# Kernel tuning notes

Measured on AMD Instinct MI355X. Metric: run time of the kernel, lower is better.

## Reference

```python
import jax, jax.numpy as jnp
import numpy as np

HID = 128      # hidden_dim
NR = 8         # num_radial
MAXL = 4       # max_angular -> 2*MAXL+1 = 9 circular harmonic features
CUT = 10.0     # cutoff
EDGE_IN = 2 * HID + NR + (2 * MAXL + 1)  # 273


def setup_inputs() -> dict:
    key = jax.random.key(0)
    ks = jax.random.split(key, 16)
    B, N = 2, 512

    def rn(k, shape, scale=0.05):
        return jax.random.normal(k, shape, dtype=jnp.float32) * scale

    return {
        "h": rn(ks[0], (B, N, HID), 1.0),
        "pos": rn(ks[1], (B, N, 2), 2.0),
        "vel": rn(ks[2], (B, N, 2), 1.0),
        # edge_net: Linear(273,256) -> SiLU -> Linear(256,128)
        "ew1": rn(ks[3], (EDGE_IN, 2 * HID)), "eb1": jnp.zeros(2 * HID, jnp.float32),
        "ew2": rn(ks[4], (2 * HID, HID)), "eb2": jnp.zeros(HID, jnp.float32),
        # coord_net: Linear(128,128) -> SiLU -> Linear(128,1)
        "cw1": rn(ks[5], (HID, HID)), "cb1": jnp.zeros(HID, jnp.float32),
        "cw2": rn(ks[6], (HID, 1)), "cb2": jnp.zeros(1, jnp.float32),
        # node_net: Linear(256,128) -> SiLU -> Linear(128,128)
        "nw1": rn(ks[7], (2 * HID, HID)), "nb1": jnp.zeros(HID, jnp.float32),
        "nw2": rn(ks[8], (HID, HID)), "nb2": jnp.zeros(HID, jnp.float32),
        # LayerNorm
        "ln_g": jnp.ones(HID, jnp.float32), "ln_b": jnp.zeros(HID, jnp.float32),
    }


def reference(h, pos, vel, ew1, eb1, ew2, eb2, cw1, cb1, cw2, cb2,
              nw1, nb1, nw2, nb2, ln_g, ln_b):
    B, N, _ = h.shape
    # all-pairs geometry: [B, N, N, 2]
    pos_diff = pos[:, :, None, :] - pos[:, None, :, :]
    dist = jnp.sqrt(jnp.sum(pos_diff * pos_diff, axis=-1))        # [B,N,N]
    direction = pos_diff / (dist[..., None] + 1e-8)

    # Gaussian radial basis on [0, cutoff]
    centers = jnp.linspace(0.0, CUT, NR).astype(h.dtype)
    width = CUT / NR
    radial = jnp.exp(-jnp.square((dist[..., None] - centers) / width))  # [B,N,N,NR]

    # smooth cosine cutoff
    cutoff = jnp.where(dist < CUT, 0.5 * (jnp.cos(jnp.pi * dist / CUT) + 1.0), 0.0)
    cutoff = cutoff[..., None]                                     # [B,N,N,1]

    # circular harmonics: [1, cos(m t), sin(m t)] m=1..MAXL -> 9 features
    theta = jnp.arctan2(direction[..., 1], direction[..., 0])
    m = jnp.arange(1, MAXL + 1, dtype=h.dtype)
    mt = theta[..., None] * m
    angular = jnp.concatenate(
        [jnp.ones_like(theta)[..., None], jnp.cos(mt), jnp.sin(mt)], axis=-1)

    h_i = jnp.broadcast_to(h[:, :, None, :], (B, N, N, HID))
    h_j = jnp.broadcast_to(h[:, None, :, :], (B, N, N, HID))
    edge_input = jnp.concatenate([h_i, h_j, radial, angular], axis=-1)  # [B,N,N,273]

    # edge MLP (dropout = identity in eval)
    e = jax.nn.silu(edge_input @ ew1 + eb1) @ ew2 + eb2            # [B,N,N,HID]
    e = e * cutoff

    # coordinate weights and position/velocity updates
    cw = (jax.nn.silu(e @ cw1 + cb1) @ cw2 + cb2)[..., 0]          # [B,N,N]
    upd = jnp.sum(pos_diff * cw[..., None], axis=2)                # [B,N,2]
    pos_out = pos + upd
    vel_out = vel + 0.1 * upd

    # message aggregation + node update
    msg_agg = jnp.sum(e, axis=2)                                   # [B,N,HID]
    node_input = jnp.concatenate([h, msg_agg], axis=-1)
    h_new = jax.nn.silu(node_input @ nw1 + nb1) @ nw2 + nb2

    # residual + LayerNorm
    x = h + h_new
    mu = jnp.mean(x, axis=-1, keepdims=True)
    var = jnp.var(x, axis=-1, keepdims=True)
    h_out = (x - mu) / jnp.sqrt(var + 1e-5) * ln_g + ln_b
    return h_out, pos_out, vel_out
```

## Files before the change

kernel.cpp:

```cpp
#include <hip/hip_runtime.h>
#include <math.h>

#define HID 128
#define NN 512
#define NNODE 1024
#define CUTR 10.0f

#define WS_A    0
#define WS_N1T  262144
#define WS_N2T  294912
#define WS_B12  393216
#define SBMT_OFF  786688
#define SE2T_OFF  (SBMT_OFF + 262144)
#define SW12T_OFF (SE2T_OFF + 32768)
#define SW1G_OFF  (SW12T_OFF + 32768)

#define OUT_POS 131072
#define OUT_VEL 133120

typedef __attribute__((ext_vector_type(8)))  short short8;
typedef __attribute__((ext_vector_type(4)))  unsigned short ushort4v;
typedef __attribute__((ext_vector_type(8)))  __bf16 bf16x8;
typedef __attribute__((ext_vector_type(16))) float float16;

__device__ __forceinline__ float silu_f(float x) {
  return x * __builtin_amdgcn_rcpf(1.f + __expf(-x));
}
__device__ __forceinline__ short f2bf(float x) {
  return __builtin_bit_cast(short, (__bf16)x);
}
__device__ __forceinline__ float bf2f(unsigned short u) {
  union { unsigned u; float f; } v; v.u = ((unsigned)u) << 16;
  return v.f;
}
__device__ __forceinline__ bf16x8 as_bf(short8 s) {
  return __builtin_bit_cast(bf16x8, s);
}
__device__ __forceinline__ float16 zero16() {
  float16 z;
#pragma unroll
  for (int r = 0; r < 16; ++r) z[r] = 0.f;
  return z;
}

__global__ __launch_bounds__(256)
void k01_prep(const float* __restrict__ h, const float* __restrict__ ew1,
              const float* __restrict__ eb1, const float* __restrict__ ew2,
              const float* __restrict__ cw1, const float* __restrict__ eb2,
              const float* __restrict__ nw1, const float* __restrict__ nw2,
              float* __restrict__ ws, unsigned short* __restrict__ wsU) {
  int blk = blockIdx.x;
  int t = threadIdx.x;
  if (blk < 1024) {
    __shared__ float sh_h[HID];
    const int node = blk;
    if (t < HID) sh_h[t] = h[node*HID + t];
    __syncthreads();
    const int c = t;
    float a = eb1[c] + ew1[264*256 + c];
    float bm = 0.f;
#pragma unroll 8
    for (int k = 0; k < HID; ++k) {
      float hk = sh_h[k];
      a  += hk * ew1[k*256 + c];
      bm += hk * ew1[(128+k)*256 + c];
    }
    ws[WS_A + node*256 + c] = a;
    const int b = node >> 9, j = node & 511;
    const int chunk = j >> 5, jr = j & 31;
    const int e = jr & 3, hlw = (jr >> 2) & 1, g = jr >> 3;
    wsU[SBMT_OFF + b*131072 + chunk*8192 + g*2048 + (c*2 + hlw)*4 + e] =
        (unsigned short)f2bf(bm);
  } else {
    int idx = (blk - 1024) * 256 + t;
    if (idx < 32768) {
      int d = idx & 127, cp = idx >> 7;
      float s = 0.f;
#pragma unroll 4
      for (int c = 0; c < 128; ++c) s += ew2[cp*128 + c] * cw1[c*128 + d];
      int sg = cp >> 4, hlw = (cp >> 3) & 1, e = cp & 7;
      wsU[SW12T_OFF + sg*2048 + d*16 + hlw*8 + e] = (unsigned short)f2bf(s);
    } else if (idx < 65536) {
      int i2 = idx - 32768; int c = i2 >> 8, k = i2 & 255;
      wsU[SE2T_OFF + c*256 + k] = (unsigned short)f2bf(ew2[k*HID + c]);
    } else if (idx < 69632) {
      int i3 = idx - 65536; int c = i3 >> 4, f = i3 & 15;
      int row = (f < 8) ? (256 + f) : (257 + f);
      wsU[SW1G_OFF + c*16 + f] = (unsigned short)f2bf(ew1[row*256 + c]);
    } else if (idx < 69760) {
      int d = idx - 69632;
      float s = 0.f;
#pragma unroll 4
      for (int c = 0; c < 128; ++c) s += eb2[c] * cw1[c*128 + d];
      ws[WS_B12 + d] = s;
    } else if (idx < 102528) {
      int i4 = idx - 69760; int d = i4 >> 8, k = i4 & 255;
      ws[WS_N1T + d*256 + k] = nw1[k*HID + d];
    } else if (idx < 118912) {
      int i5 = idx - 102528; int d = i5 >> 7, k = i5 & 127;
      ws[WS_N2T + d*128 + k] = nw2[k*HID + d];
    }
  }
}

__global__ __launch_bounds__(256)
void k3_edge(const float* __restrict__ pos, const float* __restrict__ vel,
             const float* __restrict__ h,
             const float* __restrict__ cb1, const float* __restrict__ cw2,
             const float* __restrict__ cb2, const float* __restrict__ eb2,
             const float* __restrict__ nb1, const float* __restrict__ nb2,
             const float* __restrict__ lng, const float* __restrict__ lnb,
             float* __restrict__ ws, float* __restrict__ out) {
  const short* wsS = (const short*)ws;
  const unsigned short* wsU = (const unsigned short*)ws;
  __shared__ __align__(16) short shH[2][32*256];
  __shared__ float shsum[256];
  __shared__ float shred[12];
  __shared__ float4 shTbl[128];
  __shared__ __align__(16) float2 shPos[NN];
  __shared__ float shCut[32];

  const int t = threadIdx.x;
  const int w = t >> 6, l = t & 63, lo = l & 31, hl = l >> 5, hl4 = hl * 4;
  const int node = blockIdx.x;
  const int b = node >> 9;
  const int bN = b * NN;

  const bf16x8 wg0 = as_bf(*(const short8*)(wsS + SW1G_OFF + (64*w + lo)*16 + hl*8));
  const bf16x8 wg1 = as_bf(*(const short8*)(wsS + SW1G_OFF + (64*w + 32 + lo)*16 + hl*8));

  const float a0   = ws[WS_A + node*256 + 64*w + lo];
  const float a1   = ws[WS_A + node*256 + 64*w + 32 + lo];
  const float cb2c16 = cb2[0] * (16.f/128.f);
  const float pix  = pos[node*2], piy = pos[node*2+1];

  ((float4*)shPos)[t] = ((const float4*)(pos + 2*bN))[t];
  if (t < 128) shTbl[t] = make_float4(ws[WS_B12 + t], cb1[t], cw2[t], 0.f);
  __syncthreads();

  float hs0 = 0.f, hs1 = 0.f;
  float cs = 0.f;
  float S = 0.f, SX = 0.f, SY = 0.f;
  float cutv, pjx, pjy;
  float cutv_n, pjx_n, pjy_n;

  auto phase1 = [&](int jbw, int bufsel) {
    const int jb = jbw & (NN - 1);
    const int chunk = jb >> 5;
    const float2 pj = shPos[jb + lo];
    pjx_n = pj.x; pjy_n = pj.y;
    const float dx = pix - pjx_n, dy = piy - pjy_n;
    const float d = sqrtf(dx*dx + dy*dy);
    cutv_n = (d < CUTR) ? 0.5f*(__cosf((float)M_PI*(1.f/CUTR)*d) + 1.f) : 0.f;
    if (jbw >= NN) cutv_n = 0.f;
    if (hl == 0) shCut[lo] = cutv_n;
    short8 gs;
    if (hl == 0) {
#pragma unroll
      for (int k = 0; k < 8; ++k) {
        float ctr = (CUTR * (float)k) / 7.0f;
        float tt = (d - ctr) * 0.8f;
        gs[k] = f2bf(__expf(-tt*tt));
      }
    } else {
      float invd = __builtin_amdgcn_rcpf(d + 1e-8f);
      float c1 = dx * invd, s1 = dy * invd;
      if (d == 0.f) { c1 = 1.f; s1 = 0.f; }
      float c2 = c1*c1 - s1*s1, s2 = 2.f*s1*c1;
      float c3 = c2*c1 - s2*s1, s3 = s2*c1 + c2*s1;
      float c4 = c3*c1 - s3*s1, s4 = s3*c1 + c3*s1;
      gs[0]=f2bf(c1); gs[1]=f2bf(c2); gs[2]=f2bf(c3); gs[3]=f2bf(c4);
      gs[4]=f2bf(s1); gs[5]=f2bf(s2); gs[6]=f2bf(s3); gs[7]=f2bf(s4);
    }
    const bf16x8 gf = as_bf(gs);
    short* shb = &shH[bufsel][0];
#pragma unroll
    for (int ct = 0; ct < 2; ++ct) {
      const int colg = 64*w + 32*ct + lo;
      const float av = ct ? a1 : a0;
      const unsigned short* bt =
          wsU + SBMT_OFF + b*131072 + chunk*8192 + (colg*2 + hl)*4;
      float16 ci;
#pragma unroll
      for (int g = 0; g < 4; ++g) {
        ushort4v v4 = *(const ushort4v*)(bt + g*2048);
        ci[4*g+0] = bf2f(v4[0]) + av;
        ci[4*g+1] = bf2f(v4[1]) + av;
        ci[4*g+2] = bf2f(v4[2]) + av;
        ci[4*g+3] = bf2f(v4[3]) + av;
      }
      ci = __builtin_amdgcn_mfma_f32_32x32x16_bf16(gf, ct ? wg1 : wg0, ci, 0, 0, 0);
      const int ck = colg >> 3;
      float hacc = 0.f;
#pragma unroll
      for (int r = 0; r < 16; ++r) {
        int row = (r&3) + 8*(r>>2) + hl4;
        float sv = silu_f(ci[r]);
        hacc += shCut[row] * sv;
        shb[row*256 + (((ck ^ row) & 31) << 3) + (colg & 7)] = f2bf(sv);
      }
      if (ct) hs1 += hacc; else hs0 += hacc;
    }
  };

  phase1(0, 0);
  cutv = cutv_n; pjx = pjx_n; pjy = pjy_n;
  __syncthreads();

  for (int k = 0; k < 16; ++k) {
    cs += cutv;

    float16 acc2 = zero16();
    {
      const short* wp = wsS + SW12T_OFF + (32*w + lo)*16 + hl*8;
      const short* shb = &shH[k & 1][0];
#pragma unroll 4
      for (int s = 0; s < 16; ++s) {
        bf16x8 wv = as_bf(*(const short8*)(wp + s*2048));
        const int ck = 2*s + hl;
        bf16x8 af = as_bf(*(const short8*)(shb + lo*256 + (((ck ^ lo) & 31) << 3)));
        acc2 = __builtin_amdgcn_mfma_f32_32x32x16_bf16(wv, af, acc2, 0, 0, 0);
      }
    }

    phase1((k + 1) * 32, (k + 1) & 1);

    {
      float psum = 0.f;
#pragma unroll
      for (int r = 0; r < 16; ++r) {
        const float4 cst = shTbl[32*w + (r&3) + 8*(r>>2) + hl4];
        psum += silu_f(cutv * (acc2[r] + cst.x) + cst.y) * cst.z;
      }
      psum += cb2c16;
      S += psum;
      SX += psum * pjx;
      SY += psum * pjy;
    }

    cutv = cutv_n; pjx = pjx_n; pjy = pjy_n;
    __syncthreads();
  }

  hs0 += __shfl_xor(hs0, 32);
  hs1 += __shfl_xor(hs1, 32);
  if (hl == 0) {
    shsum[64*w + lo] = hs0;
    shsum[64*w + 32 + lo] = hs1;
  }

  float cutsum = cs;
#pragma unroll
  for (int m = 1; m < 32; m <<= 1) cutsum += __shfl_xor(cutsum, m, 32);

#pragma unroll
  for (int off = 32; off > 0; off >>= 1) {
    S  += __shfl_xor(S, off);
    SX += __shfl_xor(SX, off);
    SY += __shfl_xor(SY, off);
  }
  if (l == 0) { shred[w] = S; shred[4 + w] = SX; shred[8 + w] = SY; }
  __syncthreads();

  float* shIn  = (float*)&shH[0][0];
  float* shHid = shIn + 256;
  float* pm    = (float*)&shH[1][0];
  const int d  = t & 127, half = t >> 7;

  {
    const short* er = wsS + SE2T_OFF + d*256 + half*128;
    const float* ss = shsum + half*128;
    float m = 0.f;
#pragma unroll 4
    for (int kk = 0; kk < 16; ++kk) {
      short8 v = *(const short8*)(er + kk*8);
      const float4 s0 = *(const float4*)(ss + kk*8);
      const float4 s1 = *(const float4*)(ss + kk*8 + 4);
      m += bf2f((unsigned short)v[0])*s0.x + bf2f((unsigned short)v[1])*s0.y
         + bf2f((unsigned short)v[2])*s0.z + bf2f((unsigned short)v[3])*s0.w
         + bf2f((unsigned short)v[4])*s1.x + bf2f((unsigned short)v[5])*s1.y
         + bf2f((unsigned short)v[6])*s1.z + bf2f((unsigned short)v[7])*s1.w;
    }
    pm[t] = m;
  }
  if (t == 0) {
    float St  = shred[0] + shred[1] + shred[2]  + shred[3];
    float SXt = shred[4] + shred[5] + shred[6]  + shred[7];
    float SYt = shred[8] + shred[9] + shred[10] + shred[11];
    float updx = pix*St - SXt, updy = piy*St - SYt;
    out[OUT_POS + node*2+0] = pix + updx;
    out[OUT_POS + node*2+1] = piy + updy;
    out[OUT_VEL + node*2+0] = vel[node*2+0] + 0.1f*updx;
    out[OUT_VEL + node*2+1] = vel[node*2+1] + 0.1f*updy;
  }
  __syncthreads();

  if (t < HID) {
    shIn[t]       = h[node*HID + t];
    shIn[HID + t] = pm[t] + pm[t + 128] + eb2[t] * cutsum;
  }
  __syncthreads();

  {
    const float* wr = ws + WS_N1T + d*256 + half*128;
    const float* si = shIn + half*128;
    float s = 0.f;
#pragma unroll 4
    for (int kk = 0; kk < 32; ++kk) {
      float4 wv = *(const float4*)(wr + kk*4);
      float4 iv = *(const float4*)(si + kk*4);
      s += wv.x*iv.x + wv.y*iv.y + wv.z*iv.z + wv.w*iv.w;
    }
    __syncthreads();
    pm[t] = s;
  }
  __syncthreads();
  if (t < HID) shHid[t] = silu_f(nb1[t] + pm[t] + pm[t + 128]);
  __syncthreads();

  {
    const float* wr = ws + WS_N2T + d*128 + half*64;
    const float* si = shHid + half*64;
    float s = 0.f;
#pragma unroll 4
    for (int kk = 0; kk < 16; ++kk) {
      float4 wv = *(const float4*)(wr + kk*4);
      float4 iv = *(const float4*)(si + kk*4);
      s += wv.x*iv.x + wv.y*iv.y + wv.z*iv.z + wv.w*iv.w;
    }
    pm[t] = s;
  }
  __syncthreads();

  float x = 0.f;
  if (t < HID) {
    x = shIn[t] + nb2[t] + pm[t] + pm[t + 128];
    float v1 = x, v2 = x*x;
#pragma unroll
    for (int off = 32; off > 0; off >>= 1) {
      v1 += __shfl_down(v1, off);
      v2 += __shfl_down(v2, off);
    }
    if (l == 0) { shred[w] = v1; shred[2 + w] = v2; }
  }
  __syncthreads();
  if (t < HID) {
    float mu  = (shred[0] + shred[1]) * (1.f/HID);
    float var = (shred[2] + shred[3]) * (1.f/HID) - mu*mu;
    float inv = 1.f / sqrtf(var + 1e-5f);
    out[node*HID + t] = (x - mu) * inv * lng[t] + lnb[t];
  }
}

extern "C" void kernel_launch(void* const* d_in, const int* in_sizes, int n_in,
                              void* d_out, int out_size, void* d_ws, size_t ws_size,
                              hipStream_t stream) {
  (void)in_sizes; (void)n_in; (void)out_size; (void)ws_size;
  const float* h   = (const float*)d_in[0];
  const float* pos = (const float*)d_in[1];
  const float* vel = (const float*)d_in[2];
  const float* ew1 = (const float*)d_in[3];
  const float* eb1 = (const float*)d_in[4];
  const float* ew2 = (const float*)d_in[5];
  const float* eb2 = (const float*)d_in[6];
  const float* cw1 = (const float*)d_in[7];
  const float* cb1 = (const float*)d_in[8];
  const float* cw2 = (const float*)d_in[9];
  const float* cb2 = (const float*)d_in[10];
  const float* nw1 = (const float*)d_in[11];
  const float* nb1 = (const float*)d_in[12];
  const float* nw2 = (const float*)d_in[13];
  const float* nb2 = (const float*)d_in[14];
  const float* lng = (const float*)d_in[15];
  const float* lnb = (const float*)d_in[16];
  float* out = (float*)d_out;
  float* ws  = (float*)d_ws;
  unsigned short* wsU = (unsigned short*)d_ws;

  hipLaunchKernelGGL(k01_prep, dim3(1489), dim3(256), 0, stream,
                     h, ew1, eb1, ew2, cw1, eb2, nw1, nw2, ws, wsU);
  hipLaunchKernelGGL(k3_edge, dim3(NNODE), dim3(256), 0, stream,
                     pos, vel, h, cb1, cw2, cb2, eb2,
                     nb1, nb2, lng, lnb, ws, out);
}
```

Measured before the change: 263.1 us.

## Compute per-node edge-layer projections in prep kernel with split-bf16 MFMA

The prep kernel's per-node projection of h through the first edge-layer weights used one block per node with scalar FP32 loops. It now uses 128 blocks in which each wave computes a 32x32 output tile with bf16 MFMA instructions. Each operand is split into high and low bf16 parts and three products are summed to approximate FP32 accuracy. This cuts the prep grid from 1489 to 593 blocks and reduces redundant weight reads, at the cost of small precision differences and a more intricate output layout mapping.

```diff
diff --git a/kernel.cpp b/kernel.cpp
--- a/kernel.cpp
+++ b/kernel.cpp
@@ -51,28 +51,58 @@
               float* __restrict__ ws, unsigned short* __restrict__ wsU) {
   int blk = blockIdx.x;
   int t = threadIdx.x;
-  if (blk < 1024) {
-    __shared__ float sh_h[HID];
-    const int node = blk;
-    if (t < HID) sh_h[t] = h[node*HID + t];
-    __syncthreads();
-    const int c = t;
-    float a = eb1[c] + ew1[264*256 + c];
-    float bm = 0.f;
-#pragma unroll 8
-    for (int k = 0; k < HID; ++k) {
-      float hk = sh_h[k];
-      a  += hk * ew1[k*256 + c];
-      bm += hk * ew1[(128+k)*256 + c];
-    }
-    ws[WS_A + node*256 + c] = a;
-    const int b = node >> 9, j = node & 511;
-    const int chunk = j >> 5, jr = j & 31;
-    const int e = jr & 3, hlw = (jr >> 2) & 1, g = jr >> 3;
-    wsU[SBMT_OFF + b*131072 + chunk*8192 + g*2048 + (c*2 + hlw)*4 + e] =
-        (unsigned short)f2bf(bm);
+  if (blk < 128) {
+    const int w = t >> 6, l = t & 63, lo = l & 31, hl = l >> 5;
+    const int tile  = blk * 4 + w;
+    const int nbase = (tile >> 4) * 32;
+    const int ubase = (tile & 15) * 32;
+    const bool isA  = (ubase < 256);
+    const int krow0 = isA ? 0 : 128;
+    const int ucol  = (ubase & 255) + lo;
+
+    float16 acc = zero16();
+    const float* hrow = h + (nbase + lo) * HID;
+#pragma unroll
+    for (int s = 0; s < 8; ++s) {
+      const float* hp = hrow + 16 * s + hl * 8;
+      float4 h0 = *(const float4*)(hp);
+      float4 h1 = *(const float4*)(hp + 4);
+      float av[8] = {h0.x, h0.y, h0.z, h0.w, h1.x, h1.y, h1.z, h1.w};
+      short8 ah, al;
+#pragma unroll
+      for (int e = 0; e < 8; ++e) {
+        ah[e] = f2bf(av[e]);
+        al[e] = f2bf(av[e] - bf2f((unsigned short)ah[e]));
+      }
+      short8 bh, bl;
+#pragma unroll
+      for (int e = 0; e < 8; ++e) {
+        float x = ew1[(krow0 + 16*s + hl*8 + e) * 256 + ucol];
+        bh[e] = f2bf(x);
+        bl[e] = f2bf(x - bf2f((unsigned short)bh[e]));
+      }
+      acc = __builtin_amdgcn_mfma_f32_32x32x16_bf16(as_bf(ah), as_bf(bh), acc, 0, 0, 0);
+      acc = __builtin_amdgcn_mfma_f32_32x32x16_bf16(as_bf(ah), as_bf(bl), acc, 0, 0, 0);
+      acc = __builtin_amdgcn_mfma_f32_32x32x16_bf16(as_bf(al), as_bf(bh), acc, 0, 0, 0);
+    }
+
+    if (isA) {
+      const float bias = eb1[ucol] + ew1[264*256 + ucol];
+#pragma unroll
+      for (int r = 0; r < 16; ++r) {
+        const int n = (r & 3) + 8 * (r >> 2) + 4 * hl;
+        ws[WS_A + (nbase + n) * 256 + ucol] = acc[r] + bias;
+      }
+    } else {
+      const int bb = nbase >> 9;
+      const int chunk = (nbase & 511) >> 5;
+      const int base = SBMT_OFF + bb*131072 + chunk*8192 + (ucol*2 + hl)*4;
+#pragma unroll
+      for (int r = 0; r < 16; ++r)
+        wsU[base + (r >> 2) * 2048 + (r & 3)] = (unsigned short)f2bf(acc[r]);
+    }
   } else {
-    int idx = (blk - 1024) * 256 + t;
+    int idx = (blk - 128) * 256 + t;
     if (idx < 32768) {
       int d = idx & 127, cp = idx >> 7;
       float s = 0.f;
@@ -377,7 +407,7 @@
   float* ws  = (float*)d_ws;
   unsigned short* wsU = (unsigned short*)d_ws;
 
-  hipLaunchKernelGGL(k01_prep, dim3(1489), dim3(256), 0, stream,
+  hipLaunchKernelGGL(k01_prep, dim3(593), dim3(256), 0, stream,
                      h, ew1, eb1, ew2, cw1, eb2, nw1, nw2, ws, wsU);
   hipLaunchKernelGGL(k3_edge, dim3(NNODE), dim3(256), 0, stream,
                      pos, vel, h, cb1, cw2, cb2, eb2,
```

Result: no change. 259.2 us (-1.5%).
